# Performance work log

Hardware: AMD Instinct MI355X
Metric: run time of the kernel (lower is better)

Reference implementation:

```python
import jax, jax.numpy as jnp
import numpy as np

B, M = 128, 1024
D_Z, D_PHI = 1024, 512
H1, H2 = 512, 512


def setup_inputs() -> dict:
    key = jax.random.key(0)
    ks = jax.random.split(key, 8)
    s1 = 1.0 / np.sqrt(D_Z + D_PHI)
    s2 = 1.0 / np.sqrt(H1)
    s3 = 1.0 / np.sqrt(H2)
    return {
        "g_q": jax.random.normal(ks[0], (B, D_Z), jnp.float32),
        "Phi": jax.random.normal(ks[1], (M, D_PHI), jnp.float32),
        "W1": jax.random.normal(ks[2], (D_Z + D_PHI, H1), jnp.float32) * s1,
        "b1": jnp.zeros((H1,), jnp.float32),
        "W2": jax.random.normal(ks[3], (H1, H2), jnp.float32) * s2,
        "b2": jnp.zeros((H2,), jnp.float32),
        "W3": jax.random.normal(ks[4], (H2, 1), jnp.float32) * s3,
        "b3": jnp.zeros((1,), jnp.float32),
    }


def reference(g_q, Phi, W1, b1, W2, b2, W3, b3):
    # net(cat([z_exp, phi_exp])) == (g_q @ W1[:d_z]) broadcast-summed with
    # (Phi @ W1[d_z:]) -- identical math, avoids materializing [B, M, d_z+d_phi].
    d_z = g_q.shape[1]
    hz = g_q @ W1[:d_z]          # [B, H1]
    hp = Phi @ W1[d_z:]          # [M, H1]
    h = hz[:, None, :] + hp[None, :, :] + b1      # [B, M, H1]
    h = jax.nn.gelu(h, approximate=False)         # torch GELU is exact erf form
    h = jax.nn.gelu(h @ W2 + b2, approximate=False)  # [B, M, H2]
    u = h @ W3 + b3                                # [B, M, 1]
    return u[..., 0]                               # [B, M]
```

## Files before the change

### kernel.cpp

```cpp
#include <hip/hip_runtime.h>
#include <hip/hip_bf16.h>


typedef __bf16 bf16x8 __attribute__((ext_vector_type(8)));
typedef float  f32x4  __attribute__((ext_vector_type(4)));
typedef float  f32x2  __attribute__((ext_vector_type(2)));

__device__ __forceinline__ f32x2 gelu_pk(f32x2 x) {
    f32x2 t = x * x;
    f32x2 p = __builtin_elementwise_fma(t, f32x2{0.1029436f, 0.1029436f},
                                        f32x2{2.3022082f, 2.3022082f});
    f32x2 a = p * x;
    f32x2 e;
    e.x = __builtin_amdgcn_exp2f(a.x);
    e.y = __builtin_amdgcn_exp2f(a.y);
    f32x2 d = e + f32x2{1.f, 1.f};
    f32x2 r;
    r.x = __builtin_amdgcn_rcpf(d.x);
    r.y = __builtin_amdgcn_rcpf(d.y);
    return __builtin_elementwise_fma(-x, r, x);
}

__device__ __forceinline__ unsigned int pack_bf16x2(float a, float b) {
    __hip_bfloat162 h = __float22bfloat162_rn(make_float2(a, b));
    return *reinterpret_cast<unsigned int*>(&h);
}
__device__ __forceinline__ float bf_lo(unsigned int u) {
    return __builtin_bit_cast(float, u << 16);
}
__device__ __forceinline__ float bf_hi(unsigned int u) {
    return __builtin_bit_cast(float, u & 0xffff0000u);
}

__global__ __launch_bounds__(256) void wcast_kernel(
    const float* __restrict__ W1, const float* __restrict__ W2,
    unsigned short* __restrict__ W1F, unsigned short* __restrict__ W2F)
{
    __shared__ float tr[64 * 68];
    const int t = threadIdx.x;
    const int id = blockIdx.x;

    const float* src;
    unsigned short* dst;
    int kt, nt;
    if (id < 64) { src = W2; dst = W2F; kt = id >> 3; nt = id & 7; }
    else         { src = W1; dst = W1F; kt = (id - 64) >> 3; nt = (id - 64) & 7; }
    const int k0 = kt * 64, n0 = nt * 64;

    {
        int r = t >> 2, c16 = (t & 3) * 16;
        #pragma unroll
        for (int q = 0; q < 4; ++q)
            *(float4*)&tr[r * 68 + c16 + q * 4] =
                *(const float4*)&src[(k0 + r) * 512 + n0 + c16 + q * 4];
    }
    __syncthreads();
    const int nl = t >> 2, kc16 = (t & 3) * 16;
    unsigned int pk[8];
    #pragma unroll
    for (int i = 0; i < 8; ++i) {
        float f0 = tr[(kc16 + 2 * i    ) * 68 + nl];
        float f1 = tr[(kc16 + 2 * i + 1) * 68 + nl];
        pk[i] = pack_bf16x2(f0, f1);
    }
    const int n  = n0 + nl;
    const int nf = n >> 4;
    #pragma unroll
    for (int h = 0; h < 2; ++h) {
        int kbase = k0 + kc16 + h * 8;
        int kc = kbase >> 5;
        int k8 = (kbase >> 3) & 3;
        int lane = (n & 15) + 16 * k8;
        uint4 v = h ? make_uint4(pk[4], pk[5], pk[6], pk[7])
                    : make_uint4(pk[0], pk[1], pk[2], pk[3]);
        *(uint4*)&dst[(unsigned)((kc * 32 + nf) * 512 + lane * 8)] = v;
    }
}

__global__ __launch_bounds__(512) void l1_kernel(
    const float* __restrict__ g_q, const float* __restrict__ Phi,
    const unsigned short* __restrict__ W1F, const float* __restrict__ b1,
    float* __restrict__ hzb, unsigned short* __restrict__ hpb)
{
    __shared__ __align__(16) unsigned short lA[64 * 64];

    const int t = threadIdx.x;
    const int w = t >> 6;
    const int l = t & 63;
    const int bi = blockIdx.x;
    const bool is_hz = bi < 2;
    const int r0 = is_hz ? bi * 64 : (bi - 2) * 64;
    const int ld = is_hz ? 1024 : 512;
    const int nkt = is_hz ? 16 : 8;
    const int kcb = is_hz ? 0 : 32;
    const float* src = is_hz ? g_q : Phi;

    f32x4 acc[4][4];
    #pragma unroll
    for (int a = 0; a < 4; ++a)
        #pragma unroll
        for (int bf = 0; bf < 4; ++bf)
            acc[a][bf] = f32x4{0.f, 0.f, 0.f, 0.f};

    const int arow = t >> 3;
    const int ac   = t & 7;
    const float* srow = src + (unsigned)(r0 + arow) * ld;
    const unsigned int awoff = (unsigned)(arow * 128 + ((ac ^ (arow & 7)) << 4));

    #pragma unroll 1
    for (int kt = 0; kt < nkt; ++kt) {
        uint4 breg[2][4];
        #pragma unroll
        for (int kk = 0; kk < 2; ++kk)
            #pragma unroll
            for (int bf = 0; bf < 4; ++bf)
                breg[kk][bf] = *(const uint4*)
                    &W1F[(unsigned)(((kcb + kt * 2 + kk) * 32 + w * 4 + bf) * 512 + l * 8)];

        {
            float4 p0 = *(const float4*)&srow[kt * 64 + ac * 8];
            float4 p1 = *(const float4*)&srow[kt * 64 + ac * 8 + 4];
            uint4 pk;
            pk.x = pack_bf16x2(p0.x, p0.y);
            pk.y = pack_bf16x2(p0.z, p0.w);
            pk.z = pack_bf16x2(p1.x, p1.y);
            pk.w = pack_bf16x2(p1.z, p1.w);
            *(uint4*)((char*)lA + awoff) = pk;
        }
        __syncthreads();

        #pragma unroll
        for (int kk = 0; kk < 2; ++kk) {
            const int cch = kk * 4 + (l >> 4);
            bf16x8 af[4];
            #pragma unroll
            for (int a = 0; a < 4; ++a) {
                int row = 16 * a + (l & 15);
                unsigned off = (unsigned)(row * 128 + ((cch ^ (row & 7)) << 4));
                af[a] = __builtin_bit_cast(bf16x8, *(const uint4*)((const char*)lA + off));
            }
            #pragma unroll
            for (int bf = 0; bf < 4; ++bf) {
                bf16x8 bfr = __builtin_bit_cast(bf16x8, breg[kk][bf]);
                #pragma unroll
                for (int a = 0; a < 4; ++a)
                    acc[a][bf] = __builtin_amdgcn_mfma_f32_16x16x32_bf16(
                        af[a], bfr, acc[a][bf], 0, 0, 0);
            }
        }
        __syncthreads();
    }

    const int cl = l & 15, rq = (l >> 4) * 4;
    #pragma unroll
    for (int bf = 0; bf < 4; ++bf) {
        int n = w * 64 + 16 * bf + cl;
        if (is_hz) {
            float bb = b1[n];
            #pragma unroll
            for (int a = 0; a < 4; ++a)
                #pragma unroll
                for (int r = 0; r < 4; ++r)
                    hzb[(unsigned)(r0 + 16 * a + rq + r) * 512 + n] = acc[a][bf][r] + bb;
        } else {
            #pragma unroll
            for (int a = 0; a < 4; ++a)
                #pragma unroll
                for (int r = 0; r < 4; ++r) {
                    __hip_bfloat16 v = __float2bfloat16(acc[a][bf][r]);
                    hpb[(unsigned)(r0 + 16 * a + rq + r) * 512 + n] =
                        *reinterpret_cast<unsigned short*>(&v);
                }
        }
    }
}

__global__ __launch_bounds__(512, 2) void fused_kernel(
    const float* __restrict__ hzb, const unsigned short* __restrict__ hpb,
    const unsigned short* __restrict__ W2F,
    const float* __restrict__ b2, const float* __restrict__ W3,
    const float* __restrict__ b3, float* __restrict__ out)
{
    __shared__ __align__(16) unsigned short lA[2 * 64 * 64];
    __shared__ __align__(16) unsigned short hstage[2 * 64 * 64];
    __shared__ __align__(16) float lhz[512];
    __shared__ float lred[8][64];

    const int t = threadIdx.x;
    const int w = __builtin_amdgcn_readfirstlane(t >> 6);
    const int l = t & 63;
    const int r0 = blockIdx.x * 64;
    const int b  = r0 >> 10;
    const int m0 = r0 & 1023;

    f32x4 acc[4][4];
    #pragma unroll
    for (int a = 0; a < 4; ++a)
        #pragma unroll
        for (int bf = 0; bf < 4; ++bf)
            acc[a][bf] = f32x4{0.f, 0.f, 0.f, 0.f};

    const int arow = t >> 3;
    const int ac   = t & 7;
    const unsigned short* hprow = hpb + (unsigned)(m0 + arow) * 512;
    const float4* lhz4 = (const float4*)lhz;
    const unsigned int awoff = (unsigned)(arow * 128 + ((ac ^ (arow & 7)) << 4));
    const unsigned int hoff  = (unsigned)(t * 16);

    auto HPSTAGE = [&](int kt, int buf) {
        __builtin_amdgcn_global_load_lds(
            (const __attribute__((address_space(1))) void*)(hprow + kt * 64 + ac * 8),
            (__attribute__((address_space(3))) void*)((char*)hstage + buf * 8192 + hoff),
            16, 0, 0);
    };

    auto AGEN = [&](int kt, int abuf) {
        uint4 hv = *(const uint4*)((const char*)hstage + (kt & 1) * 8192 + hoff);
        const int kb = kt * 64 + ac * 8;
        float4 z0 = lhz4[kb >> 2];
        float4 z1 = lhz4[(kb >> 2) + 1];
        f32x2 g0 = gelu_pk(f32x2{bf_lo(hv.x), bf_hi(hv.x)} + f32x2{z0.x, z0.y});
        f32x2 g1 = gelu_pk(f32x2{bf_lo(hv.y), bf_hi(hv.y)} + f32x2{z0.z, z0.w});
        f32x2 g2 = gelu_pk(f32x2{bf_lo(hv.z), bf_hi(hv.z)} + f32x2{z1.x, z1.y});
        f32x2 g3 = gelu_pk(f32x2{bf_lo(hv.w), bf_hi(hv.w)} + f32x2{z1.z, z1.w});
        uint4 pk;
        pk.x = pack_bf16x2(g0.x, g0.y);
        pk.y = pack_bf16x2(g1.x, g1.y);
        pk.z = pack_bf16x2(g2.x, g2.y);
        pk.w = pack_bf16x2(g3.x, g3.y);
        *(uint4*)((char*)lA + (unsigned)(abuf * 8192) + awoff) = pk;
    };

    HPSTAGE(0, 0);
    HPSTAGE(1, 1);
    lhz[t] = hzb[b * 512 + t];
    __syncthreads();
    AGEN(0, 0);
    __syncthreads();

    #pragma unroll 2
    for (int kt = 0; kt < 8; ++kt) {
        if (kt < 6) HPSTAGE(kt + 2, kt & 1);

        uint4 breg[2][4];
        #pragma unroll
        for (int kk = 0; kk < 2; ++kk)
            #pragma unroll
            for (int bf = 0; bf < 4; ++bf)
                breg[kk][bf] = *(const uint4*)
                    &W2F[(unsigned)(((kt * 2 + kk) * 32 + w * 4 + bf) * 512 + l * 8)];

        if (kt < 7) AGEN(kt + 1, (kt + 1) & 1);

        const char* abase = (const char*)lA + (kt & 1) * 8192;
        #pragma unroll
        for (int kk = 0; kk < 2; ++kk) {
            const int cch = kk * 4 + (l >> 4);
            bf16x8 af[4];
            #pragma unroll
            for (int a = 0; a < 4; ++a) {
                int row = 16 * a + (l & 15);
                unsigned off = (unsigned)(row * 128 + ((cch ^ (row & 7)) << 4));
                af[a] = __builtin_bit_cast(bf16x8, *(const uint4*)(abase + off));
            }
            #pragma unroll
            for (int bf = 0; bf < 4; ++bf) {
                bf16x8 bfr = __builtin_bit_cast(bf16x8, breg[kk][bf]);
                #pragma unroll
                for (int a = 0; a < 4; ++a)
                    acc[a][bf] = __builtin_amdgcn_mfma_f32_16x16x32_bf16(
                        af[a], bfr, acc[a][bf], 0, 0, 0);
            }
        }

        __syncthreads();
    }

    float b2v[4], w3v[4];
    #pragma unroll
    for (int bf = 0; bf < 4; ++bf) {
        int n = w * 64 + 16 * bf + (l & 15);
        b2v[bf] = b2[n];
        w3v[bf] = W3[n];
    }
    f32x2 ps[4][2];
    #pragma unroll
    for (int a = 0; a < 4; ++a) {
        ps[a][0] = f32x2{0.f, 0.f};
        ps[a][1] = f32x2{0.f, 0.f};
    }

    #pragma unroll
    for (int bf = 0; bf < 4; ++bf) {
        const f32x2 b2p = {b2v[bf], b2v[bf]};
        const f32x2 w3p = {w3v[bf], w3v[bf]};
        #pragma unroll
        for (int a = 0; a < 4; ++a) {
            f32x2 xlo = f32x2{acc[a][bf][0], acc[a][bf][1]} + b2p;
            f32x2 xhi = f32x2{acc[a][bf][2], acc[a][bf][3]} + b2p;
            ps[a][0] = __builtin_elementwise_fma(gelu_pk(xlo), w3p, ps[a][0]);
            ps[a][1] = __builtin_elementwise_fma(gelu_pk(xhi), w3p, ps[a][1]);
        }
    }

    float psum[4][4];
    #pragma unroll
    for (int a = 0; a < 4; ++a) {
        psum[a][0] = ps[a][0].x; psum[a][1] = ps[a][0].y;
        psum[a][2] = ps[a][1].x; psum[a][3] = ps[a][1].y;
    }

    #pragma unroll
    for (int a = 0; a < 4; ++a)
        #pragma unroll
        for (int r = 0; r < 4; ++r) {
            float v = psum[a][r];
            v += __shfl_xor(v, 1);
            v += __shfl_xor(v, 2);
            v += __shfl_xor(v, 4);
            v += __shfl_xor(v, 8);
            psum[a][r] = v;
        }

    if ((l & 15) == 0) {
        int gb = (l >> 4) * 4;
        #pragma unroll
        for (int a = 0; a < 4; ++a)
            #pragma unroll
            for (int r = 0; r < 4; ++r)
                lred[w][16 * a + gb + r] = psum[a][r];
    }
    __syncthreads();
    if (t < 64) {
        float s = b3[0];
        #pragma unroll
        for (int ww = 0; ww < 8; ++ww) s += lred[ww][t];
        out[r0 + t] = s;
    }
}

extern "C" void kernel_launch(void* const* d_in, const int* in_sizes, int n_in,
                              void* d_out, int out_size, void* d_ws, size_t ws_size,
                              hipStream_t stream) {
    (void)in_sizes; (void)n_in; (void)out_size; (void)ws_size;
    const float* g_q = (const float*)d_in[0];
    const float* Phi = (const float*)d_in[1];
    const float* W1  = (const float*)d_in[2];
    const float* b1  = (const float*)d_in[3];
    const float* W2  = (const float*)d_in[4];
    const float* b2  = (const float*)d_in[5];
    const float* W3  = (const float*)d_in[6];
    const float* b3  = (const float*)d_in[7];
    float* out = (float*)d_out;

    char* ws = (char*)d_ws;
    float*          hzb = (float*)ws;
    unsigned short* hpb = (unsigned short*)(ws + 262144);
    unsigned short* W2F = (unsigned short*)(ws + 1310720);
    unsigned short* W1F = (unsigned short*)(ws + 1835008);

    hipLaunchKernelGGL(wcast_kernel, dim3(256), dim3(256), 0, stream,
                       W1, W2, W1F, W2F);
    hipLaunchKernelGGL(l1_kernel, dim3(18), dim3(512), 0, stream,
                       g_q, Phi, W1F, b1, hzb, hpb);
    hipLaunchKernelGGL(fused_kernel, dim3(2048), dim3(512), 0, stream,
                       hzb, hpb, W2F, b2, W3, b3, out);
}
```

Baseline: 115.5 us.

## Deepen LDS ring to four slots and sync once per two k-tiles

Grows the hp staging buffer and the GELU'd A-tile buffer from two slots to four. The main loop now handles two k-tiles per iteration with a single __syncthreads, instead of one barrier per tile. Prefetch distance for hp rows goes from two to four tiles, and two A tiles are generated ahead during the prologue. This removes half the barriers and gives memory loads more time to arrive. In exchange, LDS use per block roughly doubles to about 66 KB, which could limit occupancy at the requested two blocks per CU, and register pressure rises from the unrolled loop.

```diff
diff --git a/kernel.cpp b/kernel.cpp
--- a/kernel.cpp
+++ b/kernel.cpp
@@ -181,8 +181,8 @@
     const float* __restrict__ b2, const float* __restrict__ W3,
     const float* __restrict__ b3, float* __restrict__ out)
 {
-    __shared__ __align__(16) unsigned short lA[2 * 64 * 64];
-    __shared__ __align__(16) unsigned short hstage[2 * 64 * 64];
+    __shared__ __align__(16) unsigned short lA[4 * 64 * 64];
+    __shared__ __align__(16) unsigned short hstage[4 * 64 * 64];
     __shared__ __align__(16) float lhz[512];
     __shared__ float lred[8][64];
 
@@ -207,15 +207,16 @@
     const unsigned int awoff = (unsigned)(arow * 128 + ((ac ^ (arow & 7)) << 4));
     const unsigned int hoff  = (unsigned)(t * 16);
 
-    auto HPSTAGE = [&](int kt, int buf) {
+    auto HPSTAGE = [&](int kt) {
         __builtin_amdgcn_global_load_lds(
             (const __attribute__((address_space(1))) void*)(hprow + kt * 64 + ac * 8),
-            (__attribute__((address_space(3))) void*)((char*)hstage + buf * 8192 + hoff),
+            (__attribute__((address_space(3))) void*)
+                ((char*)hstage + (kt & 3) * 8192 + hoff),
             16, 0, 0);
     };
 
-    auto AGEN = [&](int kt, int abuf) {
-        uint4 hv = *(const uint4*)((const char*)hstage + (kt & 1) * 8192 + hoff);
+    auto AGEN = [&](int kt) {
+        uint4 hv = *(const uint4*)((const char*)hstage + (kt & 3) * 8192 + hoff);
         const int kb = kt * 64 + ac * 8;
         float4 z0 = lhz4[kb >> 2];
         float4 z1 = lhz4[(kb >> 2) + 1];
@@ -228,31 +229,20 @@
         pk.y = pack_bf16x2(g1.x, g1.y);
         pk.z = pack_bf16x2(g2.x, g2.y);
         pk.w = pack_bf16x2(g3.x, g3.y);
-        *(uint4*)((char*)lA + (unsigned)(abuf * 8192) + awoff) = pk;
+        *(uint4*)((char*)lA + (unsigned)((kt & 3) * 8192) + awoff) = pk;
     };
 
-    HPSTAGE(0, 0);
-    HPSTAGE(1, 1);
-    lhz[t] = hzb[b * 512 + t];
-    __syncthreads();
-    AGEN(0, 0);
-    __syncthreads();
-
-    #pragma unroll 2
-    for (int kt = 0; kt < 8; ++kt) {
-        if (kt < 6) HPSTAGE(kt + 2, kt & 1);
-
-        uint4 breg[2][4];
+    auto BLOADK = [&](int kt, uint4 breg[2][4]) {
         #pragma unroll
         for (int kk = 0; kk < 2; ++kk)
             #pragma unroll
             for (int bf = 0; bf < 4; ++bf)
                 breg[kk][bf] = *(const uint4*)
                     &W2F[(unsigned)(((kt * 2 + kk) * 32 + w * 4 + bf) * 512 + l * 8)];
-
-        if (kt < 7) AGEN(kt + 1, (kt + 1) & 1);
-
-        const char* abase = (const char*)lA + (kt & 1) * 8192;
+    };
+
+    auto MFMA_KT = [&](int kt, uint4 breg[2][4]) {
+        const char* abase = (const char*)lA + (kt & 3) * 8192;
         #pragma unroll
         for (int kk = 0; kk < 2; ++kk) {
             const int cch = kk * 4 + (l >> 4);
@@ -272,6 +262,28 @@
                         af[a], bfr, acc[a][bf], 0, 0, 0);
             }
         }
+    };
+
+    HPSTAGE(0); HPSTAGE(1); HPSTAGE(2); HPSTAGE(3);
+    lhz[t] = hzb[b * 512 + t];
+    __syncthreads();
+    AGEN(0); AGEN(1);
+    __syncthreads();
+
+    uint4 breg[2][4];
+    #pragma unroll
+    for (int i = 0; i < 4; ++i) {
+        const int kt0 = 2 * i, kt1 = 2 * i + 1;
+
+        if (i < 2) { HPSTAGE(kt0 + 4); HPSTAGE(kt1 + 4); }
+
+        BLOADK(kt0, breg);
+        if (i < 3) AGEN(kt0 + 2);
+        MFMA_KT(kt0, breg);
+
+        BLOADK(kt1, breg);
+        if (i < 3) AGEN(kt1 + 2);
+        MFMA_KT(kt1, breg);
 
         __syncthreads();
     }
```

New measurement: 125.6 us. +8.7%, slower.

## Pre-cast g_q and Phi to MFMA fragment layout in cast kernel, drop LDS staging in l1

Applied to the files above, without the earlier changes.

The cast kernel now also converts g_q and Phi to bf16 and writes them in MFMA fragment order, using 160 extra blocks. The layer-1 GEMM then loads A fragments straight from global memory instead of staging them through swizzled LDS, which removes both __syncthreads per k-step and lets the loop unroll by 2. The cost is one more global write and read round trip for the activations, plus extra workspace, in exchange for a sync-free inner loop in a kernel that runs only 18 blocks.

```diff
diff --git a/kernel.cpp b/kernel.cpp
--- a/kernel.cpp
+++ b/kernel.cpp
@@ -34,66 +34,95 @@
 
 __global__ __launch_bounds__(256) void wcast_kernel(
     const float* __restrict__ W1, const float* __restrict__ W2,
-    unsigned short* __restrict__ W1F, unsigned short* __restrict__ W2F)
+    const float* __restrict__ g_q, const float* __restrict__ Phi,
+    unsigned short* __restrict__ W1F, unsigned short* __restrict__ W2F,
+    unsigned short* __restrict__ gqF, unsigned short* __restrict__ PhiF)
 {
     __shared__ float tr[64 * 68];
     const int t = threadIdx.x;
     const int id = blockIdx.x;
 
-    const float* src;
-    unsigned short* dst;
-    int kt, nt;
-    if (id < 64) { src = W2; dst = W2F; kt = id >> 3; nt = id & 7; }
-    else         { src = W1; dst = W1F; kt = (id - 64) >> 3; nt = (id - 64) & 7; }
-    const int k0 = kt * 64, n0 = nt * 64;
-
-    {
-        int r = t >> 2, c16 = (t & 3) * 16;
-        #pragma unroll
-        for (int q = 0; q < 4; ++q)
-            *(float4*)&tr[r * 68 + c16 + q * 4] =
-                *(const float4*)&src[(k0 + r) * 512 + n0 + c16 + q * 4];
-    }
-    __syncthreads();
-    const int nl = t >> 2, kc16 = (t & 3) * 16;
-    unsigned int pk[8];
-    #pragma unroll
-    for (int i = 0; i < 8; ++i) {
-        float f0 = tr[(kc16 + 2 * i    ) * 68 + nl];
-        float f1 = tr[(kc16 + 2 * i + 1) * 68 + nl];
-        pk[i] = pack_bf16x2(f0, f1);
-    }
-    const int n  = n0 + nl;
-    const int nf = n >> 4;
-    #pragma unroll
-    for (int h = 0; h < 2; ++h) {
-        int kbase = k0 + kc16 + h * 8;
-        int kc = kbase >> 5;
-        int k8 = (kbase >> 3) & 3;
-        int lane = (n & 15) + 16 * k8;
-        uint4 v = h ? make_uint4(pk[4], pk[5], pk[6], pk[7])
-                    : make_uint4(pk[0], pk[1], pk[2], pk[3]);
-        *(uint4*)&dst[(unsigned)((kc * 32 + nf) * 512 + lane * 8)] = v;
+    if (id < 256) {
+        const float* src;
+        unsigned short* dst;
+        int kt, nt;
+        if (id < 64) { src = W2; dst = W2F; kt = id >> 3; nt = id & 7; }
+        else         { src = W1; dst = W1F; kt = (id - 64) >> 3; nt = (id - 64) & 7; }
+        const int k0 = kt * 64, n0 = nt * 64;
+
+        {
+            int r = t >> 2, c16 = (t & 3) * 16;
+            #pragma unroll
+            for (int q = 0; q < 4; ++q)
+                *(float4*)&tr[r * 68 + c16 + q * 4] =
+                    *(const float4*)&src[(k0 + r) * 512 + n0 + c16 + q * 4];
+        }
+        __syncthreads();
+        const int nl = t >> 2, kc16 = (t & 3) * 16;
+        unsigned int pk[8];
+        #pragma unroll
+        for (int i = 0; i < 8; ++i) {
+            float f0 = tr[(kc16 + 2 * i    ) * 68 + nl];
+            float f1 = tr[(kc16 + 2 * i + 1) * 68 + nl];
+            pk[i] = pack_bf16x2(f0, f1);
+        }
+        const int n  = n0 + nl;
+        const int nf = n >> 4;
+        #pragma unroll
+        for (int h = 0; h < 2; ++h) {
+            int kbase = k0 + kc16 + h * 8;
+            int kc = kbase >> 5;
+            int k8 = (kbase >> 3) & 3;
+            int lane = (n & 15) + 16 * k8;
+            uint4 v = h ? make_uint4(pk[4], pk[5], pk[6], pk[7])
+                        : make_uint4(pk[0], pk[1], pk[2], pk[3]);
+            *(uint4*)&dst[(unsigned)((kc * 32 + nf) * 512 + lane * 8)] = v;
+        }
+    } else {
+        const float* src;
+        unsigned short* dst;
+        int rt, ktile, ld, nrf;
+        if (id < 288) { src = g_q; dst = gqF;  int q = id - 256; rt = q >> 4; ktile = q & 15; ld = 1024; nrf = 8; }
+        else          { src = Phi; dst = PhiF; int q = id - 288; rt = q >> 3; ktile = q & 7;  ld = 512;  nrf = 64; }
+        const int r0 = rt * 64, kb0 = ktile * 64;
+        const int l = t & 63;
+        #pragma unroll
+        for (int i = 0; i < 2; ++i) {
+            int f   = (t >> 6) + 4 * i;
+            int rf  = f & 3;
+            int kcl = f >> 2;
+            int row = r0 + rf * 16 + (l & 15);
+            int k   = kb0 + kcl * 32 + (l >> 4) * 8;
+            float4 p0 = *(const float4*)&src[row * ld + k];
+            float4 p1 = *(const float4*)&src[row * ld + k + 4];
+            uint4 v;
+            v.x = pack_bf16x2(p0.x, p0.y);
+            v.y = pack_bf16x2(p0.z, p0.w);
+            v.z = pack_bf16x2(p1.x, p1.y);
+            v.w = pack_bf16x2(p1.z, p1.w);
+            int kc = (kb0 >> 5) + kcl;
+            int rfg = (r0 >> 4) + rf;
+            *(uint4*)&dst[(unsigned)((kc * nrf + rfg) * 512 + l * 8)] = v;
+        }
     }
 }
 
 __global__ __launch_bounds__(512) void l1_kernel(
-    const float* __restrict__ g_q, const float* __restrict__ Phi,
+    const unsigned short* __restrict__ gqF, const unsigned short* __restrict__ PhiF,
     const unsigned short* __restrict__ W1F, const float* __restrict__ b1,
     float* __restrict__ hzb, unsigned short* __restrict__ hpb)
 {
-    __shared__ __align__(16) unsigned short lA[64 * 64];
-
     const int t = threadIdx.x;
     const int w = t >> 6;
     const int l = t & 63;
     const int bi = blockIdx.x;
     const bool is_hz = bi < 2;
-    const int r0 = is_hz ? bi * 64 : (bi - 2) * 64;
-    const int ld = is_hz ? 1024 : 512;
+    const int r0  = is_hz ? bi * 64 : (bi - 2) * 64;
     const int nkt = is_hz ? 16 : 8;
     const int kcb = is_hz ? 0 : 32;
-    const float* src = is_hz ? g_q : Phi;
+    const int nrf = is_hz ? 8 : 64;
+    const int rb0 = r0 >> 4;
+    const unsigned short* AF = is_hz ? gqF : PhiF;
 
     f32x4 acc[4][4];
     #pragma unroll
@@ -102,53 +131,29 @@
         for (int bf = 0; bf < 4; ++bf)
             acc[a][bf] = f32x4{0.f, 0.f, 0.f, 0.f};
 
-    const int arow = t >> 3;
-    const int ac   = t & 7;
-    const float* srow = src + (unsigned)(r0 + arow) * ld;
-    const unsigned int awoff = (unsigned)(arow * 128 + ((ac ^ (arow & 7)) << 4));
-
-    #pragma unroll 1
+    #pragma unroll 2
     for (int kt = 0; kt < nkt; ++kt) {
-        uint4 breg[2][4];
-        #pragma unroll
-        for (int kk = 0; kk < 2; ++kk)
+        #pragma unroll
+        for (int kk = 0; kk < 2; ++kk) {
+            const int kc = kt * 2 + kk;
+            uint4 afr[4], bfr[4];
+            #pragma unroll
+            for (int a = 0; a < 4; ++a)
+                afr[a] = *(const uint4*)
+                    &AF[(unsigned)((kc * nrf + rb0 + a) * 512 + l * 8)];
             #pragma unroll
             for (int bf = 0; bf < 4; ++bf)
-                breg[kk][bf] = *(const uint4*)
-                    &W1F[(unsigned)(((kcb + kt * 2 + kk) * 32 + w * 4 + bf) * 512 + l * 8)];
-
-        {
-            float4 p0 = *(const float4*)&srow[kt * 64 + ac * 8];
-            float4 p1 = *(const float4*)&srow[kt * 64 + ac * 8 + 4];
-            uint4 pk;
-            pk.x = pack_bf16x2(p0.x, p0.y);
-            pk.y = pack_bf16x2(p0.z, p0.w);
-            pk.z = pack_bf16x2(p1.x, p1.y);
-            pk.w = pack_bf16x2(p1.z, p1.w);
-            *(uint4*)((char*)lA + awoff) = pk;
-        }
-        __syncthreads();
-
-        #pragma unroll
-        for (int kk = 0; kk < 2; ++kk) {
-            const int cch = kk * 4 + (l >> 4);
-            bf16x8 af[4];
-            #pragma unroll
-            for (int a = 0; a < 4; ++a) {
-                int row = 16 * a + (l & 15);
-                unsigned off = (unsigned)(row * 128 + ((cch ^ (row & 7)) << 4));
-                af[a] = __builtin_bit_cast(bf16x8, *(const uint4*)((const char*)lA + off));
-            }
+                bfr[bf] = *(const uint4*)
+                    &W1F[(unsigned)(((kcb + kc) * 32 + w * 4 + bf) * 512 + l * 8)];
             #pragma unroll
             for (int bf = 0; bf < 4; ++bf) {
-                bf16x8 bfr = __builtin_bit_cast(bf16x8, breg[kk][bf]);
+                bf16x8 bb = __builtin_bit_cast(bf16x8, bfr[bf]);
                 #pragma unroll
                 for (int a = 0; a < 4; ++a)
                     acc[a][bf] = __builtin_amdgcn_mfma_f32_16x16x32_bf16(
-                        af[a], bfr, acc[a][bf], 0, 0, 0);
+                        __builtin_bit_cast(bf16x8, afr[a]), bb, acc[a][bf], 0, 0, 0);
             }
         }
-        __syncthreads();
     }
 
     const int cl = l & 15, rq = (l >> 4) * 4;
@@ -354,15 +359,17 @@
     float* out = (float*)d_out;
 
     char* ws = (char*)d_ws;
-    float*          hzb = (float*)ws;
-    unsigned short* hpb = (unsigned short*)(ws + 262144);
-    unsigned short* W2F = (unsigned short*)(ws + 1310720);
-    unsigned short* W1F = (unsigned short*)(ws + 1835008);
-
-    hipLaunchKernelGGL(wcast_kernel, dim3(256), dim3(256), 0, stream,
-                       W1, W2, W1F, W2F);
+    float*          hzb  = (float*)ws;
+    unsigned short* hpb  = (unsigned short*)(ws + 262144);
+    unsigned short* W2F  = (unsigned short*)(ws + 1310720);
+    unsigned short* W1F  = (unsigned short*)(ws + 1835008);
+    unsigned short* gqF  = (unsigned short*)(ws + 3407872);
+    unsigned short* PhiF = (unsigned short*)(ws + 3670016);
+
+    hipLaunchKernelGGL(wcast_kernel, dim3(416), dim3(256), 0, stream,
+                       W1, W2, g_q, Phi, W1F, W2F, gqF, PhiF);
     hipLaunchKernelGGL(l1_kernel, dim3(18), dim3(512), 0, stream,
-                       g_q, Phi, W1F, b1, hzb, hpb);
+                       gqF, PhiF, W1F, b1, hzb, hpb);
     hipLaunchKernelGGL(fused_kernel, dim3(2048), dim3(512), 0, stream,
                        hzb, hpb, W2F, b2, W3, b3, out);
 }
```

New measurement: 120.8 us. 1.05x slower.

## Merge weight cast and layer-1 GEMM into one prep kernel reading fp32 W1 directly

Applied to the files above, without the earlier changes.

Replaces the separate W1/W2 cast kernel and the layer-1 GEMM kernel with a single prep kernel. Blocks 0-63 cast W2 into the MFMA fragment layout. The remaining 72 blocks compute hz/hp rows in 16-row tiles, loading fp32 W1 directly with strided scalar loads and converting it to bf16 in registers. This drops one launch, the W1F workspace round-trip and the serial dependency between the kernels. The cost is uncoalesced W1 reads with no shared-memory reuse across row tiles, and more blocks each re-reading all of W1.

```diff
diff --git a/kernel.cpp b/kernel.cpp
--- a/kernel.cpp
+++ b/kernel.cpp
@@ -32,145 +32,108 @@
     return __builtin_bit_cast(float, u & 0xffff0000u);
 }
 
-__global__ __launch_bounds__(256) void wcast_kernel(
-    const float* __restrict__ W1, const float* __restrict__ W2,
-    unsigned short* __restrict__ W1F, unsigned short* __restrict__ W2F)
+__global__ __launch_bounds__(512) void prep_kernel(
+    const float* __restrict__ g_q, const float* __restrict__ Phi,
+    const float* __restrict__ W1, const float* __restrict__ b1,
+    const float* __restrict__ W2,
+    float* __restrict__ hzb, unsigned short* __restrict__ hpb,
+    unsigned short* __restrict__ W2F)
 {
     __shared__ float tr[64 * 68];
     const int t = threadIdx.x;
     const int id = blockIdx.x;
 
-    const float* src;
-    unsigned short* dst;
-    int kt, nt;
-    if (id < 64) { src = W2; dst = W2F; kt = id >> 3; nt = id & 7; }
-    else         { src = W1; dst = W1F; kt = (id - 64) >> 3; nt = (id - 64) & 7; }
-    const int k0 = kt * 64, n0 = nt * 64;
-
-    {
-        int r = t >> 2, c16 = (t & 3) * 16;
-        #pragma unroll
-        for (int q = 0; q < 4; ++q)
-            *(float4*)&tr[r * 68 + c16 + q * 4] =
-                *(const float4*)&src[(k0 + r) * 512 + n0 + c16 + q * 4];
-    }
-    __syncthreads();
-    const int nl = t >> 2, kc16 = (t & 3) * 16;
-    unsigned int pk[8];
-    #pragma unroll
-    for (int i = 0; i < 8; ++i) {
-        float f0 = tr[(kc16 + 2 * i    ) * 68 + nl];
-        float f1 = tr[(kc16 + 2 * i + 1) * 68 + nl];
-        pk[i] = pack_bf16x2(f0, f1);
-    }
-    const int n  = n0 + nl;
-    const int nf = n >> 4;
-    #pragma unroll
-    for (int h = 0; h < 2; ++h) {
-        int kbase = k0 + kc16 + h * 8;
-        int kc = kbase >> 5;
-        int k8 = (kbase >> 3) & 3;
-        int lane = (n & 15) + 16 * k8;
-        uint4 v = h ? make_uint4(pk[4], pk[5], pk[6], pk[7])
-                    : make_uint4(pk[0], pk[1], pk[2], pk[3]);
-        *(uint4*)&dst[(unsigned)((kc * 32 + nf) * 512 + lane * 8)] = v;
-    }
-}
-
-__global__ __launch_bounds__(512) void l1_kernel(
-    const float* __restrict__ g_q, const float* __restrict__ Phi,
-    const unsigned short* __restrict__ W1F, const float* __restrict__ b1,
-    float* __restrict__ hzb, unsigned short* __restrict__ hpb)
-{
-    __shared__ __align__(16) unsigned short lA[64 * 64];
-
-    const int t = threadIdx.x;
-    const int w = t >> 6;
-    const int l = t & 63;
-    const int bi = blockIdx.x;
-    const bool is_hz = bi < 2;
-    const int r0 = is_hz ? bi * 64 : (bi - 2) * 64;
-    const int ld = is_hz ? 1024 : 512;
-    const int nkt = is_hz ? 16 : 8;
-    const int kcb = is_hz ? 0 : 32;
-    const float* src = is_hz ? g_q : Phi;
-
-    f32x4 acc[4][4];
-    #pragma unroll
-    for (int a = 0; a < 4; ++a)
-        #pragma unroll
-        for (int bf = 0; bf < 4; ++bf)
-            acc[a][bf] = f32x4{0.f, 0.f, 0.f, 0.f};
-
-    const int arow = t >> 3;
-    const int ac   = t & 7;
-    const float* srow = src + (unsigned)(r0 + arow) * ld;
-    const unsigned int awoff = (unsigned)(arow * 128 + ((ac ^ (arow & 7)) << 4));
-
-    #pragma unroll 1
-    for (int kt = 0; kt < nkt; ++kt) {
-        uint4 breg[2][4];
-        #pragma unroll
-        for (int kk = 0; kk < 2; ++kk)
-            #pragma unroll
-            for (int bf = 0; bf < 4; ++bf)
-                breg[kk][bf] = *(const uint4*)
-                    &W1F[(unsigned)(((kcb + kt * 2 + kk) * 32 + w * 4 + bf) * 512 + l * 8)];
-
+    if (id < 64) {
+        const int kt = id >> 3, nt = id & 7;
+        const int k0 = kt * 64, n0 = nt * 64;
         {
-            float4 p0 = *(const float4*)&srow[kt * 64 + ac * 8];
-            float4 p1 = *(const float4*)&srow[kt * 64 + ac * 8 + 4];
-            uint4 pk;
-            pk.x = pack_bf16x2(p0.x, p0.y);
-            pk.y = pack_bf16x2(p0.z, p0.w);
-            pk.z = pack_bf16x2(p1.x, p1.y);
-            pk.w = pack_bf16x2(p1.z, p1.w);
-            *(uint4*)((char*)lA + awoff) = pk;
+            int row = t >> 3, col = (t & 7) * 8;
+            *(float4*)&tr[row * 68 + col] =
+                *(const float4*)&W2[(k0 + row) * 512 + n0 + col];
+            *(float4*)&tr[row * 68 + col + 4] =
+                *(const float4*)&W2[(k0 + row) * 512 + n0 + col + 4];
         }
         __syncthreads();
-
-        #pragma unroll
-        for (int kk = 0; kk < 2; ++kk) {
-            const int cch = kk * 4 + (l >> 4);
-            bf16x8 af[4];
-            #pragma unroll
-            for (int a = 0; a < 4; ++a) {
-                int row = 16 * a + (l & 15);
-                unsigned off = (unsigned)(row * 128 + ((cch ^ (row & 7)) << 4));
-                af[a] = __builtin_bit_cast(bf16x8, *(const uint4*)((const char*)lA + off));
+        const int nl = t >> 3, kc16 = (t & 7) * 8;
+        unsigned int pk[4];
+        #pragma unroll
+        for (int i = 0; i < 4; ++i) {
+            float f0 = tr[(kc16 + 2 * i    ) * 68 + nl];
+            float f1 = tr[(kc16 + 2 * i + 1) * 68 + nl];
+            pk[i] = pack_bf16x2(f0, f1);
+        }
+        const int n   = n0 + nl;
+        const int nf  = n >> 4;
+        const int kbase = k0 + kc16;
+        const int kc  = kbase >> 5;
+        const int k8  = (kbase >> 3) & 3;
+        const int lane = (n & 15) + 16 * k8;
+        *(uint4*)&W2F[(unsigned)((kc * 32 + nf) * 512 + lane * 8)] =
+            make_uint4(pk[0], pk[1], pk[2], pk[3]);
+    } else {
+        const int bi = id - 64;
+        const bool is_hz = bi < 8;
+        const int r0  = is_hz ? bi * 16 : (bi - 8) * 16;
+        const int ld  = is_hz ? 1024 : 512;
+        const int nkc = is_hz ? 32 : 16;
+        const int kw0 = is_hz ? 0 : 1024;
+        const float* src = is_hz ? g_q : Phi;
+
+        const int w = t >> 6;
+        const int l = t & 63;
+        const int row = r0 + (l & 15);
+        const int k8  = l >> 4;
+        const float* arow = src + (unsigned)row * ld;
+
+        f32x4 acc[4];
+        #pragma unroll
+        for (int bf = 0; bf < 4; ++bf) acc[bf] = f32x4{0.f, 0.f, 0.f, 0.f};
+
+        #pragma unroll 2
+        for (int kc = 0; kc < nkc; ++kc) {
+            const int kb = kc * 32 + k8 * 8;
+            float4 a0 = *(const float4*)&arow[kb];
+            float4 a1 = *(const float4*)&arow[kb + 4];
+            uint4 av;
+            av.x = pack_bf16x2(a0.x, a0.y);
+            av.y = pack_bf16x2(a0.z, a0.w);
+            av.z = pack_bf16x2(a1.x, a1.y);
+            av.w = pack_bf16x2(a1.z, a1.w);
+            bf16x8 af = __builtin_bit_cast(bf16x8, av);
+            #pragma unroll
+            for (int bf = 0; bf < 4; ++bf) {
+                const float* wp = &W1[(unsigned)(kw0 + kb) * 512 + w * 64 + bf * 16 + (l & 15)];
+                float b0 = wp[0],        b1v = wp[512];
+                float b2 = wp[2 * 512],  b3v = wp[3 * 512];
+                float b4 = wp[4 * 512],  b5v = wp[5 * 512];
+                float b6 = wp[6 * 512],  b7v = wp[7 * 512];
+                uint4 bv;
+                bv.x = pack_bf16x2(b0, b1v);
+                bv.y = pack_bf16x2(b2, b3v);
+                bv.z = pack_bf16x2(b4, b5v);
+                bv.w = pack_bf16x2(b6, b7v);
+                acc[bf] = __builtin_amdgcn_mfma_f32_16x16x32_bf16(
+                    af, __builtin_bit_cast(bf16x8, bv), acc[bf], 0, 0, 0);
             }
-            #pragma unroll
-            for (int bf = 0; bf < 4; ++bf) {
-                bf16x8 bfr = __builtin_bit_cast(bf16x8, breg[kk][bf]);
-                #pragma unroll
-                for (int a = 0; a < 4; ++a)
-                    acc[a][bf] = __builtin_amdgcn_mfma_f32_16x16x32_bf16(
-                        af[a], bfr, acc[a][bf], 0, 0, 0);
-            }
-        }
-        __syncthreads();
-    }
-
-    const int cl = l & 15, rq = (l >> 4) * 4;
-    #pragma unroll
-    for (int bf = 0; bf < 4; ++bf) {
-        int n = w * 64 + 16 * bf + cl;
-        if (is_hz) {
-            float bb = b1[n];
-            #pragma unroll
-            for (int a = 0; a < 4; ++a)
+        }
+
+        const int cl = l & 15, rq = (l >> 4) * 4;
+        #pragma unroll
+        for (int bf = 0; bf < 4; ++bf) {
+            int n = w * 64 + bf * 16 + cl;
+            if (is_hz) {
+                float bb = b1[n];
                 #pragma unroll
                 for (int r = 0; r < 4; ++r)
-                    hzb[(unsigned)(r0 + 16 * a + rq + r) * 512 + n] = acc[a][bf][r] + bb;
-        } else {
-            #pragma unroll
-            for (int a = 0; a < 4; ++a)
+                    hzb[(unsigned)(r0 + rq + r) * 512 + n] = acc[bf][r] + bb;
+            } else {
                 #pragma unroll
                 for (int r = 0; r < 4; ++r) {
-                    __hip_bfloat16 v = __float2bfloat16(acc[a][bf][r]);
-                    hpb[(unsigned)(r0 + 16 * a + rq + r) * 512 + n] =
+                    __hip_bfloat16 v = __float2bfloat16(acc[bf][r]);
+                    hpb[(unsigned)(r0 + rq + r) * 512 + n] =
                         *reinterpret_cast<unsigned short*>(&v);
                 }
+            }
         }
     }
 }
@@ -357,12 +320,9 @@
     float*          hzb = (float*)ws;
     unsigned short* hpb = (unsigned short*)(ws + 262144);
     unsigned short* W2F = (unsigned short*)(ws + 1310720);
-    unsigned short* W1F = (unsigned short*)(ws + 1835008);
-
-    hipLaunchKernelGGL(wcast_kernel, dim3(256), dim3(256), 0, stream,
-                       W1, W2, W1F, W2F);
-    hipLaunchKernelGGL(l1_kernel, dim3(18), dim3(512), 0, stream,
-                       g_q, Phi, W1F, b1, hzb, hpb);
+
+    hipLaunchKernelGGL(prep_kernel, dim3(136), dim3(512), 0, stream,
+                       g_q, Phi, W1, b1, W2, hzb, hpb, W2F);
     hipLaunchKernelGGL(fused_kernel, dim3(2048), dim3(512), 0, stream,
                        hzb, hpb, W2F, b2, W3, b3, out);
 }
```

Result: slower. 162.9 us (+41.0%).
